# Kernel optimization log

Hardware: AMD Instinct MI355X
Metric: run time of the kernel (lower is better)

## Reference

```python
import jax, jax.numpy as jnp
import numpy as np

NPLANETS = 10
NEDGES = NPLANETS * (NPLANETS - 1) // 2  # 45
NTIME = 100000


def _cart_to_sph(v):
    # v: [..., 3] cartesian -> [r, theta, phi]
    x, y, z = v[..., 0], v[..., 1], v[..., 2]
    r = jnp.sqrt(x * x + y * y + z * z)
    theta = jnp.arccos(jnp.clip(z / r, -1.0, 1.0))
    phi = jnp.arctan2(y, x)
    return jnp.stack([r, theta, phi], axis=-1)


def _sph_to_cart(v):
    # v: [..., 3] [r, theta, phi] -> cartesian
    r, theta, phi = v[..., 0], v[..., 1], v[..., 2]
    st = jnp.sin(theta)
    return jnp.stack([r * st * jnp.cos(phi), r * st * jnp.sin(phi), r * jnp.cos(theta)], axis=-1)


def setup_inputs() -> dict:
    key = jax.random.key(0)
    ks = jax.random.split(key, 8)
    # fully-connected upper-triangle edge list (i < j)
    s_np, r_np = np.triu_indices(NPLANETS, k=1)
    senders = jnp.asarray(s_np, dtype=jnp.int32)
    receivers = jnp.asarray(r_np, dtype=jnp.int32)
    D_V = jax.random.normal(ks[0], (NTIME * NEDGES, 3), dtype=jnp.float32)
    logm = jax.random.normal(ks[1], (NPLANETS,), dtype=jnp.float32)
    W1 = jax.random.normal(ks[2], (5, 32), dtype=jnp.float32) * 0.3
    b1 = jnp.zeros((32,), dtype=jnp.float32)
    W2 = jax.random.normal(ks[3], (32, 32), dtype=jnp.float32) * 0.2
    b2 = jnp.zeros((32,), dtype=jnp.float32)
    W3 = jax.random.normal(ks[4], (32, 3), dtype=jnp.float32) * 0.2
    b3 = jnp.zeros((3,), dtype=jnp.float32)
    return {"D_V": D_V, "logm": logm, "W1": W1, "b1": b1, "W2": W2, "b2": b2,
            "W3": W3, "b3": b3, "senders": senders, "receivers": receivers}


def reference(D_V, logm, W1, b1, W2, b2, W3, b3, senders, receivers):
    nplanets = logm.shape[0]
    nedges = senders.shape[0]
    ntime = D_V.shape[0] // nedges
    num_nodes = ntime * nplanets

    lm = jnp.clip(logm, -12.0, 12.0)
    nodes = jnp.tile(lm, ntime)[:, None]  # [ntime*nplanets, 1]

    # per-timestep node-index offsets for the replicated edge list
    offsets = jnp.repeat(jnp.arange(ntime, dtype=senders.dtype) * nplanets, nedges)
    s_g = jnp.tile(senders, ntime) + offsets    # [E]
    r_g = jnp.tile(receivers, ntime) + offsets  # [E]

    edges_sph = _cart_to_sph(D_V)  # [E, 3]
    # EdgeBlock: concat(edges, receiver_nodes, sender_nodes) -> MLP [32,32,3], tanh
    feat = jnp.concatenate([edges_sph, nodes[r_g], nodes[s_g]], axis=-1)  # [E, 5]
    h = jnp.tanh(feat @ W1 + b1)
    h = jnp.tanh(h @ W2 + b2)
    e = h @ W3 + b3  # [E, 3] spherical forces

    e_cart = _sph_to_cart(e)
    recv_sum = jax.ops.segment_sum(e_cart, r_g, num_segments=num_nodes)
    sent_sum = jax.ops.segment_sum(e_cart, s_g, num_segments=num_nodes)
    forces = recv_sum - sent_sum  # [N, 3]

    accel = forces / jnp.exp(nodes)  # broadcast over [N, 1]
    return accel.reshape(ntime, nplanets, 3)
```

## Files before the change

kernel.cpp:

```cpp
#include <hip/hip_runtime.h>
#include <hip/hip_bf16.h>
#include <math.h>

#define NP 10
#define NE 45
#define TS 16
#define EPB (TS * NE)
#define BLOCK 256
#define NCHUNK ((EPB + 63) / 64)

typedef __attribute__((ext_vector_type(8))) short short8;
typedef __attribute__((ext_vector_type(4))) float f32x4;
typedef __attribute__((ext_vector_type(2))) float f32x2;

#define C2LOG2E 2.885390081777927f
#define PI_F    3.14159265358979f
#define PIO2_F  1.57079632679490f

__device__ __forceinline__ float rcp_fast(float x) { return __builtin_amdgcn_rcpf(x); }

__device__ __forceinline__ int tanh_pair_pk(float s0, float s1) {
    f32x2 e;
    e.x = __builtin_amdgcn_exp2f(s0);
    e.y = __builtin_amdgcn_exp2f(s1);
    f32x2 f = e + 1.0f;
    float r  = rcp_fast(f.x * f.y);
    f32x2 g;
    g.x = f.y; g.y = f.x;
    f32x2 t = g * (-2.0f * r) + 1.0f;
    float2 hv; hv.x = t.x; hv.y = t.y;
    __hip_bfloat162 b = __float22bfloat162_rn(hv);
    return *(int*)&b;
}

__device__ __forceinline__ short bf16_rne(float f) {
    unsigned int u = __float_as_uint(f);
    return (short)((u + 0x7fffu + ((u >> 16) & 1u)) >> 16);
}
__device__ __forceinline__ int bf16pk2(float a, float b) {
    float2 v; v.x = a; v.y = b;
    __hip_bfloat162 t = __float22bfloat162_rn(v);
    return *(int*)&t;
}
__device__ __forceinline__ int bperm_i(int idx_bytes, int v) {
    return __builtin_amdgcn_ds_bpermute(idx_bytes, v);
}

__device__ __forceinline__ float acos_fast(float w) {
    float a = fabsf(w);
    float s = sqrtf(1.0f - a);
    float p = fmaf(a, fmaf(a, fmaf(a, -0.0187293f, 0.0742610f), -0.2121144f), 1.5707288f);
    float v = s * p;
    return (w >= 0.0f) ? v : PI_F - v;
}
__device__ __forceinline__ float atan2_fast(float y, float x) {
    float ax = fabsf(x), ay = fabsf(y);
    float mx = fmaxf(ax, ay), mn = fminf(ax, ay);
    float t  = mn * rcp_fast(mx);
    float s  = t * t;
    float p  = fmaf(s, fmaf(s, fmaf(s, fmaf(s, 0.0208351f, -0.0851330f),
                                       0.1801410f), -0.3302995f), 0.9998660f);
    float rr = p * t;
    rr = (ay > ax)   ? PIO2_F - rr : rr;
    rr = (x < 0.0f)  ? PI_F  - rr : rr;
    return __builtin_copysignf(rr, y);
}

__global__ __launch_bounds__(BLOCK, 4) void
learn_forces_kernel(const float* __restrict__ D_V, const float* __restrict__ logm,
                    const float* __restrict__ W1, const float* __restrict__ b1,
                    const float* __restrict__ W2, const float* __restrict__ b2,
                    const float* __restrict__ W3, const float* __restrict__ b3,
                    const int* __restrict__ senders, const int* __restrict__ receivers,
                    float* __restrict__ out, int ntime)
{
    __shared__ float einv[NP];
    __shared__ int   stab[NP * 9];
    __shared__ int   mpair[NE];
    __shared__ float secart[3][EPB];

    const int tid  = threadIdx.x;
    const int wv   = tid >> 6, lane = tid & 63;
    const int m    = lane & 15, q = lane >> 4;

    if (tid < NP) {
        float l = fminf(12.0f, fmaxf(-12.0f, logm[tid]));
        einv[tid] = __expf(-l);
    }
    if (tid < NE) {
        float lr = fminf(12.0f, fmaxf(-12.0f, logm[receivers[tid]]));
        float ls = fminf(12.0f, fmaxf(-12.0f, logm[senders[tid]]));
        mpair[tid] = bf16pk2(lr, ls);
    }
    if (tid < NP) {
        int cnt = 0;
        for (int e = 0; e < NE; ++e) {
            if (receivers[e] == tid) stab[tid * 9 + cnt++] =  (e + 1);
            if (senders[e]   == tid) stab[tid * 9 + cnt++] = -(e + 1);
        }
        for (; cnt < 9; ++cnt) stab[tid * 9 + cnt] = 0;
    }

    const int nm = 8 * (m >> 2) + (m & 3);
    short8 a1[2], a2[2], a3;
    f32x4  cb1[2], cb2[2], cb3;
    #pragma unroll
    for (int t = 0; t < 2; ++t) {
        const int n = nm + 4 * t;
        #pragma unroll
        for (int j = 0; j < 8; ++j) {
            int k = 8 * q + j;
            a1[t][j] = (k < 5) ? bf16_rne(W1[k * 32 + n] * C2LOG2E) : (short)0;
            a2[t][j] = bf16_rne(W2[k * 32 + n] * C2LOG2E);
        }
        #pragma unroll
        for (int r = 0; r < 4; ++r) {
            int nn = 8 * q + 4 * t + r;
            cb1[t][r] = b1[nn] * C2LOG2E;
            cb2[t][r] = b2[nn] * C2LOG2E;
        }
    }
    {
        const int c3 = m & 3;
        #pragma unroll
        for (int j = 0; j < 8; ++j)
            a3[j] = (c3 < 3) ? bf16_rne(W3[(8 * q + j) * 3 + c3]) : (short)0;
        #pragma unroll
        for (int r = 0; r < 4; ++r)
            cb3[r] = (r < 3) ? b3[r] : 0.0f;
    }

    const int bpm = m * 4;
    __syncthreads();

    const long ebase = (long)blockIdx.x * EPB;
    float xn = 1.f, yn = 0.f, zn = 0.f;
    {
        int e0i = wv * 64 + lane;
        if (e0i < EPB) {
            const float* dv = D_V + (ebase + e0i) * 3;
            xn = dv[0]; yn = dv[1]; zn = dv[2];
        }
    }

    for (int c = wv; c < NCHUNK; c += 4) {
        const int  e_loc  = c * 64 + lane;
        const bool active = e_loc < EPB;

        float x = xn, y = yn, z = zn;
        xn = 1.f; yn = 0.f; zn = 0.f;
        {
            int enx = (c + 4) * 64 + lane;
            if (c + 4 < NCHUNK && enx < EPB) {
                const float* dv = D_V + (ebase + enx) * 3;
                xn = dv[0]; yn = dv[1]; zn = dv[2];
            }
        }

        const int le = e_loc % NE;
        float ss  = fmaf(x, x, fmaf(y, y, z * z));
        float rsq = __builtin_amdgcn_rsqf(ss);
        float r   = ss * rsq;
        float zr  = fminf(1.0f, fmaxf(-1.0f, z * rsq));
        float th  = acos_fast(zr);
        float ph  = atan2_fast(y, x);

        int mp   = mpair[le];
        int p_rt = bf16pk2(r, th);
        int p_pm = (int)__builtin_amdgcn_perm(
                       (unsigned)mp, __float_as_uint(ph) + 0x8000u, 0x05040302u);
        int p_s0 = ((unsigned)mp) >> 16;

        int b0[4], b1g[4], b2g[4];
        #pragma unroll
        for (int g = 0; g < 4; ++g) {
            const int idx = bpm + g * 64;
            b0[g]  = bperm_i(idx, p_rt);
            b1g[g] = bperm_i(idx, p_pm);
            b2g[g] = bperm_i(idx, p_s0);
        }

        f32x4 d0[4], d1[4];
        #pragma unroll
        for (int g = 0; g < 4; ++g) {
            short8 bf1;
            int* bi = (int*)&bf1;
            bi[0] = b0[g]; bi[1] = b1g[g]; bi[2] = b2g[g]; bi[3] = 0;
            d0[g] = __builtin_amdgcn_mfma_f32_16x16x32_bf16(a1[0], bf1, cb1[0], 0, 0, 0);
            d1[g] = __builtin_amdgcn_mfma_f32_16x16x32_bf16(a1[1], bf1, cb1[1], 0, 0, 0);
        }

        #pragma unroll
        for (int g = 0; g < 4; ++g) {
            short8 bh;
            int* hb = (int*)&bh;
            hb[0] = tanh_pair_pk(d0[g][0], d0[g][1]);
            hb[1] = tanh_pair_pk(d0[g][2], d0[g][3]);
            hb[2] = tanh_pair_pk(d1[g][0], d1[g][1]);
            hb[3] = tanh_pair_pk(d1[g][2], d1[g][3]);
            d0[g] = __builtin_amdgcn_mfma_f32_16x16x32_bf16(a2[0], bh, cb2[0], 0, 0, 0);
            d1[g] = __builtin_amdgcn_mfma_f32_16x16x32_bf16(a2[1], bh, cb2[1], 0, 0, 0);
        }

        f32x4 d3[4];
        #pragma unroll
        for (int g = 0; g < 4; ++g) {
            short8 bh;
            int* hb = (int*)&bh;
            hb[0] = tanh_pair_pk(d0[g][0], d0[g][1]);
            hb[1] = tanh_pair_pk(d0[g][2], d0[g][3]);
            hb[2] = tanh_pair_pk(d1[g][0], d1[g][1]);
            hb[3] = tanh_pair_pk(d1[g][2], d1[g][3]);
            d3[g] = __builtin_amdgcn_mfma_f32_16x16x32_bf16(a3, bh, cb3, 0, 0, 0);
        }

        float e0a = (q & 1) ? d3[1][0] : d3[0][0], e0b = (q & 1) ? d3[3][0] : d3[2][0];
        float e1a = (q & 1) ? d3[1][1] : d3[0][1], e1b = (q & 1) ? d3[3][1] : d3[2][1];
        float e2a = (q & 1) ? d3[1][2] : d3[0][2], e2b = (q & 1) ? d3[3][2] : d3[2][2];
        float e0 = (q & 2) ? e0b : e0a;
        float e1 = (q & 2) ? e1b : e1a;
        float e2 = (q & 2) ? e2b : e2a;

        float st = __sinf(e1), ct = __cosf(e1);
        float sp = __sinf(e2), cp = __cosf(e2);
        float a  = e0 * st;
        f32x2 xy;
        {
            f32x2 cs; cs.x = cp; cs.y = sp;
            xy = cs * a;
        }
        if (active) {
            secart[0][e_loc] = xy.x;
            secart[1][e_loc] = xy.y;
            secart[2][e_loc] = e0 * ct;
        }
    }
    __syncthreads();

    const long t0g = (long)blockIdx.x * TS;
    for (int i = tid; i < TS * NP * 3; i += BLOCK) {
        int t  = i / (NP * 3);
        int pc = i - t * (NP * 3);
        int p  = pc / 3;
        int cc = pc - p * 3;
        const float* row = &secart[cc][t * NE];
        float s = 0.0f;
        #pragma unroll
        for (int j = 0; j < 9; ++j) {
            int es = stab[p * 9 + j];
            int e  = (es < 0 ? -es : es) - 1;
            float v = row[e];
            s += (es > 0) ? v : -v;
        }
        out[t0g * NP * 3 + i] = s * einv[p];
    }
}

extern "C" void kernel_launch(void* const* d_in, const int* in_sizes, int n_in,
                              void* d_out, int out_size, void* d_ws, size_t ws_size,
                              hipStream_t stream) {
    const float* D_V  = (const float*)d_in[0];
    const float* logm = (const float*)d_in[1];
    const float* W1   = (const float*)d_in[2];
    const float* b1   = (const float*)d_in[3];
    const float* W2   = (const float*)d_in[4];
    const float* b2   = (const float*)d_in[5];
    const float* W3   = (const float*)d_in[6];
    const float* b3   = (const float*)d_in[7];
    const int* senders   = (const int*)d_in[8];
    const int* receivers = (const int*)d_in[9];

    int nedges = in_sizes[8];
    int ntime  = in_sizes[0] / 3 / nedges;

    int nblocks = (ntime + TS - 1) / TS;
    learn_forces_kernel<<<nblocks, BLOCK, 0, stream>>>(
        D_V, logm, W1, b1, W2, b2, W3, b3, senders, receivers,
        (float*)d_out, ntime);
}
```

Before: 205.4 us.

## Switch edge MLP from 16x16x32 to 32x32x16 bf16 MFMA tiles

Reformulates the per-edge three-layer MLP to use 32x32x16 bf16 MFMAs, so each wave handles two 32-edge tiles with far fewer permute shuffles (3 bpermutes instead of 12). It also folds the layer-1 bias into the weight matrix through a constant-one input feature and adds the layer-3 bias after the MFMA. The aim is to reduce cross-lane shuffle overhead and MFMA instruction count. The trade-off is larger 16-float accumulators, which raise register pressure, plus a different lane-to-neuron mapping that must match the operand layout exactly.

Result: no change. 203.7 us (-0.8%).

```diff
diff --git a/kernel.cpp b/kernel.cpp
--- a/kernel.cpp
+++ b/kernel.cpp
@@ -9,13 +9,15 @@
 #define BLOCK 256
 #define NCHUNK ((EPB + 63) / 64)
 
-typedef __attribute__((ext_vector_type(8))) short short8;
-typedef __attribute__((ext_vector_type(4))) float f32x4;
-typedef __attribute__((ext_vector_type(2))) float f32x2;
+typedef __attribute__((ext_vector_type(8)))  short short8;
+typedef __attribute__((ext_vector_type(16))) float f32x16;
+typedef __attribute__((ext_vector_type(2)))  float f32x2;
 
 #define C2LOG2E 2.885390081777927f
 #define PI_F    3.14159265358979f
 #define PIO2_F  1.57079632679490f
+
+#define MFMA32(a, b, c) __builtin_amdgcn_mfma_f32_32x32x16_bf16(a, b, c, 0, 0, 0)
 
 __device__ __forceinline__ float rcp_fast(float x) { return __builtin_amdgcn_rcpf(x); }
 
@@ -81,7 +83,7 @@
 
     const int tid  = threadIdx.x;
     const int wv   = tid >> 6, lane = tid & 63;
-    const int m    = lane & 15, q = lane >> 4;
+    const int n    = lane & 31, h = lane >> 5;
 
     if (tid < NP) {
         float l = fminf(12.0f, fmaxf(-12.0f, logm[tid]));
@@ -101,36 +103,34 @@
         for (; cnt < 9; ++cnt) stab[tid * 9 + cnt] = 0;
     }
 
-    const int nm = 8 * (m >> 2) + (m & 3);
-    short8 a1[2], a2[2], a3;
-    f32x4  cb1[2], cb2[2], cb3;
+    const int nu = 16 * (n >> 4) + 8 * ((n >> 2) & 1) + 4 * ((n >> 3) & 1) + (n & 3);
+    const int c3 = n & 3;
+
+    short8 a1, a2a, a2b, a3a, a3b;
+    f32x16 cb2, zf16;
     #pragma unroll
-    for (int t = 0; t < 2; ++t) {
-        const int n = nm + 4 * t;
-        #pragma unroll
-        for (int j = 0; j < 8; ++j) {
-            int k = 8 * q + j;
-            a1[t][j] = (k < 5) ? bf16_rne(W1[k * 32 + n] * C2LOG2E) : (short)0;
-            a2[t][j] = bf16_rne(W2[k * 32 + n] * C2LOG2E);
-        }
-        #pragma unroll
-        for (int r = 0; r < 4; ++r) {
-            int nn = 8 * q + 4 * t + r;
-            cb1[t][r] = b1[nn] * C2LOG2E;
-            cb2[t][r] = b2[nn] * C2LOG2E;
-        }
-    }
-    {
-        const int c3 = m & 3;
-        #pragma unroll
-        for (int j = 0; j < 8; ++j)
-            a3[j] = (c3 < 3) ? bf16_rne(W3[(8 * q + j) * 3 + c3]) : (short)0;
-        #pragma unroll
-        for (int r = 0; r < 4; ++r)
-            cb3[r] = (r < 3) ? b3[r] : 0.0f;
-    }
-
-    const int bpm = m * 4;
+    for (int j = 0; j < 8; ++j) {
+        const int k = 8 * h + j;
+        float w1v = 0.0f;
+        if (h == 0) {
+            if (j < 5)       w1v = W1[j * 32 + nu] * C2LOG2E;
+            else if (j == 5) w1v = b1[nu] * C2LOG2E;
+        }
+        a1[j]  = bf16_rne(w1v);
+        a2a[j] = bf16_rne(W2[k * 32 + nu] * C2LOG2E);
+        a2b[j] = bf16_rne(W2[(16 + k) * 32 + nu] * C2LOG2E);
+        a3a[j] = (c3 < 3) ? bf16_rne(W3[k * 3 + c3]) : (short)0;
+        a3b[j] = (c3 < 3) ? bf16_rne(W3[(16 + k) * 3 + c3]) : (short)0;
+    }
+    #pragma unroll
+    for (int r = 0; r < 16; ++r) {
+        int neuron = (r < 8) ? (8 * h + r) : (16 + 8 * h + (r - 8));
+        cb2[r]  = b2[neuron] * C2LOG2E;
+        zf16[r] = 0.0f;
+    }
+    const float b30 = b3[0], b31 = b3[1], b32 = b3[2];
+
+    const int idxg1 = (n | 32) * 4;
     __syncthreads();
 
     const long ebase = (long)blockIdx.x * EPB;
@@ -169,65 +169,69 @@
         int p_rt = bf16pk2(r, th);
         int p_pm = (int)__builtin_amdgcn_perm(
                        (unsigned)mp, __float_as_uint(ph) + 0x8000u, 0x05040302u);
-        int p_s0 = ((unsigned)mp) >> 16;
-
-        int b0[4], b1g[4], b2g[4];
-        #pragma unroll
-        for (int g = 0; g < 4; ++g) {
-            const int idx = bpm + g * 64;
-            b0[g]  = bperm_i(idx, p_rt);
-            b1g[g] = bperm_i(idx, p_pm);
-            b2g[g] = bperm_i(idx, p_s0);
-        }
-
-        f32x4 d0[4], d1[4];
-        #pragma unroll
-        for (int g = 0; g < 4; ++g) {
-            short8 bf1;
-            int* bi = (int*)&bf1;
-            bi[0] = b0[g]; bi[1] = b1g[g]; bi[2] = b2g[g]; bi[3] = 0;
-            d0[g] = __builtin_amdgcn_mfma_f32_16x16x32_bf16(a1[0], bf1, cb1[0], 0, 0, 0);
-            d1[g] = __builtin_amdgcn_mfma_f32_16x16x32_bf16(a1[1], bf1, cb1[1], 0, 0, 0);
-        }
-
-        #pragma unroll
-        for (int g = 0; g < 4; ++g) {
-            short8 bh;
-            int* hb = (int*)&bh;
-            hb[0] = tanh_pair_pk(d0[g][0], d0[g][1]);
-            hb[1] = tanh_pair_pk(d0[g][2], d0[g][3]);
-            hb[2] = tanh_pair_pk(d1[g][0], d1[g][1]);
-            hb[3] = tanh_pair_pk(d1[g][2], d1[g][3]);
-            d0[g] = __builtin_amdgcn_mfma_f32_16x16x32_bf16(a2[0], bh, cb2[0], 0, 0, 0);
-            d1[g] = __builtin_amdgcn_mfma_f32_16x16x32_bf16(a2[1], bh, cb2[1], 0, 0, 0);
-        }
-
-        f32x4 d3[4];
-        #pragma unroll
-        for (int g = 0; g < 4; ++g) {
-            short8 bh;
-            int* hb = (int*)&bh;
-            hb[0] = tanh_pair_pk(d0[g][0], d0[g][1]);
-            hb[1] = tanh_pair_pk(d0[g][2], d0[g][3]);
-            hb[2] = tanh_pair_pk(d1[g][0], d1[g][1]);
-            hb[3] = tanh_pair_pk(d1[g][2], d1[g][3]);
-            d3[g] = __builtin_amdgcn_mfma_f32_16x16x32_bf16(a3, bh, cb3, 0, 0, 0);
-        }
-
-        float e0a = (q & 1) ? d3[1][0] : d3[0][0], e0b = (q & 1) ? d3[3][0] : d3[2][0];
-        float e1a = (q & 1) ? d3[1][1] : d3[0][1], e1b = (q & 1) ? d3[3][1] : d3[2][1];
-        float e2a = (q & 1) ? d3[1][2] : d3[0][2], e2b = (q & 1) ? d3[3][2] : d3[2][2];
-        float e0 = (q & 2) ? e0b : e0a;
-        float e1 = (q & 2) ? e1b : e1a;
-        float e2 = (q & 2) ? e2b : e2a;
+        int p_s1 = (int)(((unsigned)mp >> 16) | 0x3F800000u);
+
+        int q_rt = bperm_i(idxg1, p_rt);
+        int q_pm = bperm_i(idxg1, p_pm);
+        int q_s1 = bperm_i(idxg1, p_s1);
+
+        short8 bf0, bf1;
+        { int* b = (int*)&bf0; b[0] = p_rt; b[1] = p_pm; b[2] = p_s1; b[3] = 0; }
+        { int* b = (int*)&bf1; b[0] = q_rt; b[1] = q_pm; b[2] = q_s1; b[3] = 0; }
+
+        f32x16 dA = MFMA32(a1, bf0, zf16);
+        f32x16 dB = MFMA32(a1, bf1, zf16);
+
+        short8 hA0, hA1, hB0, hB1;
+        {
+            int* p = (int*)&hA0; int* q2 = (int*)&hA1;
+            p[0]  = tanh_pair_pk(dA[0],  dA[1]);  p[1]  = tanh_pair_pk(dA[2],  dA[3]);
+            p[2]  = tanh_pair_pk(dA[4],  dA[5]);  p[3]  = tanh_pair_pk(dA[6],  dA[7]);
+            q2[0] = tanh_pair_pk(dA[8],  dA[9]);  q2[1] = tanh_pair_pk(dA[10], dA[11]);
+            q2[2] = tanh_pair_pk(dA[12], dA[13]); q2[3] = tanh_pair_pk(dA[14], dA[15]);
+        }
+        {
+            int* p = (int*)&hB0; int* q2 = (int*)&hB1;
+            p[0]  = tanh_pair_pk(dB[0],  dB[1]);  p[1]  = tanh_pair_pk(dB[2],  dB[3]);
+            p[2]  = tanh_pair_pk(dB[4],  dB[5]);  p[3]  = tanh_pair_pk(dB[6],  dB[7]);
+            q2[0] = tanh_pair_pk(dB[8],  dB[9]);  q2[1] = tanh_pair_pk(dB[10], dB[11]);
+            q2[2] = tanh_pair_pk(dB[12], dB[13]); q2[3] = tanh_pair_pk(dB[14], dB[15]);
+        }
+        f32x16 eA = MFMA32(a2a, hA0, cb2);
+        eA        = MFMA32(a2b, hA1, eA);
+        f32x16 eB = MFMA32(a2a, hB0, cb2);
+        eB        = MFMA32(a2b, hB1, eB);
+
+        {
+            int* p = (int*)&hA0; int* q2 = (int*)&hA1;
+            p[0]  = tanh_pair_pk(eA[0],  eA[1]);  p[1]  = tanh_pair_pk(eA[2],  eA[3]);
+            p[2]  = tanh_pair_pk(eA[4],  eA[5]);  p[3]  = tanh_pair_pk(eA[6],  eA[7]);
+            q2[0] = tanh_pair_pk(eA[8],  eA[9]);  q2[1] = tanh_pair_pk(eA[10], eA[11]);
+            q2[2] = tanh_pair_pk(eA[12], eA[13]); q2[3] = tanh_pair_pk(eA[14], eA[15]);
+        }
+        {
+            int* p = (int*)&hB0; int* q2 = (int*)&hB1;
+            p[0]  = tanh_pair_pk(eB[0],  eB[1]);  p[1]  = tanh_pair_pk(eB[2],  eB[3]);
+            p[2]  = tanh_pair_pk(eB[4],  eB[5]);  p[3]  = tanh_pair_pk(eB[6],  eB[7]);
+            q2[0] = tanh_pair_pk(eB[8],  eB[9]);  q2[1] = tanh_pair_pk(eB[10], eB[11]);
+            q2[2] = tanh_pair_pk(eB[12], eB[13]); q2[3] = tanh_pair_pk(eB[14], eB[15]);
+        }
+        f32x16 oA = MFMA32(a3a, hA0, zf16);
+        oA        = MFMA32(a3b, hA1, oA);
+        f32x16 oB = MFMA32(a3a, hB0, zf16);
+        oB        = MFMA32(a3b, hB1, oB);
+
+        float e0 = (h ? oB[0] : oA[0]) + b30;
+        float e1 = (h ? oB[1] : oA[1]) + b31;
+        float e2 = (h ? oB[2] : oA[2]) + b32;
 
         float st = __sinf(e1), ct = __cosf(e1);
         float sp = __sinf(e2), cp = __cosf(e2);
-        float a  = e0 * st;
+        float am = e0 * st;
         f32x2 xy;
         {
             f32x2 cs; cs.x = cp; cs.y = sp;
-            xy = cs * a;
+            xy = cs * am;
         }
         if (active) {
             secart[0][e_loc] = xy.x;
```
